# Optimization experiments

Measured on AMD Instinct MI355X. Metric: run time of the kernel, lower is better.

Reference implementation:

```python
import jax, jax.numpy as jnp
from jax import lax
import numpy as np

N, D, K = 262144, 256, 32


def setup_inputs() -> dict:
    key = jax.random.key(0)
    k1, k2 = jax.random.split(key)
    inputs = jax.random.normal(k1, (N, D), dtype=jnp.float32)
    q_vectors = jax.random.normal(k2, (K, D), dtype=jnp.float32)
    return {"inputs": inputs, "q_vectors": q_vectors}


def reference(inputs, q_vectors):
    # Sequence of Householder reflections: x <- x - (x @ q) outer (2/||q||^2 q)
    squared_norms = jnp.sum(q_vectors ** 2, axis=-1)  # [K]

    def step(x, qn):
        q, sq = qn  # q: [D], sq: scalar
        coeff = x @ q  # [N]
        x = x - jnp.outer(coeff, (2.0 / sq) * q)  # rank-1 update, [N, D]
        return x, None

    outputs, _ = lax.scan(step, inputs, (q_vectors, squared_norms))
    logabsdet = jnp.zeros(inputs.shape[0], dtype=inputs.dtype)
    return outputs, logabsdet
```

## Files before the change

kernel.cpp:

```cpp
#include <hip/hip_runtime.h>

#define N_ROWS 262144
#define DDIM   256
#define KREF   32

typedef __attribute__((ext_vector_type(4))) float f32x4;
typedef __attribute__((ext_vector_type(8))) short bf16x8;

__device__ bf16x8 g_Vhi[2 * 8 * 64];
__device__ bf16x8 g_Vlo[2 * 8 * 64];
__device__ bf16x8 g_Uhi[16 * 64];
__device__ bf16x8 g_Ulo[16 * 64];

__device__ __forceinline__ unsigned short f2bf(float x) {
    unsigned u = __float_as_uint(x);
    u += 0x7fffu + ((u >> 16) & 1u);
    return (unsigned short)(u >> 16);
}
__device__ __forceinline__ float bf2f(unsigned short h) {
    return __uint_as_float(((unsigned)h) << 16);
}

#define QS_LD 264
#define T_LD  33
#define U_LD  36

__global__ __launch_bounds__(256)
void setup_kernel(const float* __restrict__ Q) {
    __shared__ float Qs[32 * QS_LD];
    __shared__ float G[32 * 32];
    __shared__ float T[32 * T_LD];
    __shared__ float beta[32];
    __shared__ float U[256 * U_LD];
    const int tid = threadIdx.x;

    {
        const int q  = tid >> 3;
        const int c8 = tid & 7;
        const f32x4* src = (const f32x4*)(Q + q * DDIM);
        f32x4* dst = (f32x4*)(Qs + q * QS_LD);
        #pragma unroll
        for (int i = 0; i < 8; ++i)
            dst[c8 + 8 * i] = src[c8 + 8 * i];
    }
    __syncthreads();

    for (int p = tid; p < 1024; p += 256) {
        const int i = p >> 5, j = p & 31;
        const f32x4* qi = (const f32x4*)(Qs + i * QS_LD);
        const f32x4* qj = (const f32x4*)(Qs + j * QS_LD);
        float s = 0.f;
        #pragma unroll 8
        for (int d = 0; d < 64; ++d) {
            const f32x4 a = qi[d], b = qj[d];
            s += a.x * b.x + a.y * b.y + a.z * b.z + a.w * b.w;
        }
        G[p] = s;
    }
    for (int p = tid; p < 32 * T_LD; p += 256) T[p] = 0.f;
    __syncthreads();

    if (tid < 32) beta[tid] = 2.0f / G[tid * 32 + tid];
    __syncthreads();

    for (int k = 0; k < 32; ++k) {
        if (tid < k) {
            float s = 0.f;
            for (int j = tid; j < k; ++j) s += T[tid * T_LD + j] * G[j * 32 + k];
            T[tid * T_LD + k] = -beta[k] * s;
        } else if (tid == k) {
            T[k * T_LD + k] = beta[k];
        }
        __syncthreads();
    }

    for (int p = tid; p < 256 * 32; p += 256) {
        const int d = p >> 5, k = p & 31;
        float s = 0.f;
        for (int j = k; j < 32; ++j) s += T[k * T_LD + j] * Qs[j * QS_LD + d];
        U[d * U_LD + k] = s;
    }
    __syncthreads();

    for (int e = tid; e < 2 * 8 * 64; e += 256) {
        const int lane = e & 63, c = (e >> 6) & 7, nt = e >> 9;
        const int q  = 16 * nt + (lane & 15);
        const int d0 = 32 * c + 8 * (lane >> 4);
        bf16x8 vh, vl;
        #pragma unroll
        for (int j = 0; j < 8; ++j) {
            const float x = Qs[q * QS_LD + d0 + j];
            const unsigned short h = f2bf(x);
            vh[j] = (short)h;
            vl[j] = (short)f2bf(x - bf2f(h));
        }
        g_Vhi[e] = vh; g_Vlo[e] = vl;
    }
    for (int e = tid; e < 16 * 64; e += 256) {
        const int lane = e & 63, mt = e >> 6;
        const int d  = 16 * mt + (lane & 15);
        const int k0 = 8 * (lane >> 4);
        bf16x8 uh, ul;
        #pragma unroll
        for (int j = 0; j < 8; ++j) {
            const float x = U[d * U_LD + k0 + j];
            const unsigned short h = f2bf(x);
            uh[j] = (short)h;
            ul[j] = (short)f2bf(x - bf2f(h));
        }
        g_Uhi[e] = uh; g_Ulo[e] = ul;
    }
}

__global__ __launch_bounds__(256)
void wy_kernel(const float* __restrict__ X, float* __restrict__ out) {
    __shared__ float tlds[4 * 16 * 36];

    const int tid  = threadIdx.x;
    const int wave = tid >> 6;
    const int lane = tid & 63;
    const int t = lane & 15;
    const int g = lane >> 4;

    const size_t row0 = (size_t)blockIdx.x * 64 + wave * 16;

    const float* xp = X + (row0 + t) * DDIM + 8 * g;
    f32x4 xa[16];
    #pragma unroll
    for (int c = 0; c < 8; ++c) {
        xa[2 * c]     = *(const f32x4*)(xp + 32 * c);
        xa[2 * c + 1] = *(const f32x4*)(xp + 32 * c + 4);
    }

    bf16x8 ahi[8], alo[8];
    #pragma unroll
    for (int c = 0; c < 8; ++c) {
        #pragma unroll
        for (int e = 0; e < 8; ++e) {
            const float x = (e < 4) ? xa[2 * c][e] : xa[2 * c + 1][e - 4];
            const unsigned short h = f2bf(x);
            ahi[c][e] = (short)h;
            alo[c][e] = (short)f2bf(x - bf2f(h));
        }
    }

    f32x4 acc0 = {0.f, 0.f, 0.f, 0.f};
    f32x4 acc1 = {0.f, 0.f, 0.f, 0.f};
    #pragma unroll
    for (int c = 0; c < 8; ++c) {
        const bf16x8 bh0 = g_Vhi[c * 64 + lane];
        const bf16x8 bl0 = g_Vlo[c * 64 + lane];
        const bf16x8 bh1 = g_Vhi[512 + c * 64 + lane];
        const bf16x8 bl1 = g_Vlo[512 + c * 64 + lane];
        acc0 = __builtin_amdgcn_mfma_f32_16x16x32_bf16(ahi[c], bh0, acc0, 0, 0, 0);
        acc0 = __builtin_amdgcn_mfma_f32_16x16x32_bf16(alo[c], bh0, acc0, 0, 0, 0);
        acc0 = __builtin_amdgcn_mfma_f32_16x16x32_bf16(ahi[c], bl0, acc0, 0, 0, 0);
        acc1 = __builtin_amdgcn_mfma_f32_16x16x32_bf16(ahi[c], bh1, acc1, 0, 0, 0);
        acc1 = __builtin_amdgcn_mfma_f32_16x16x32_bf16(alo[c], bh1, acc1, 0, 0, 0);
        acc1 = __builtin_amdgcn_mfma_f32_16x16x32_bf16(ahi[c], bl1, acc1, 0, 0, 0);
    }

    const float* xr = X + (row0 + t) * DDIM + 4 * g;
    f32x4 xe[16];
    #pragma unroll
    for (int mt = 0; mt < 16; ++mt)
        xe[mt] = *(const f32x4*)(xr + 16 * mt);

    float* tb = tlds + wave * (16 * 36);
    #pragma unroll
    for (int r = 0; r < 4; ++r) {
        tb[(4 * g + r) * 36 + t]      = acc0[r];
        tb[(4 * g + r) * 36 + 16 + t] = acc1[r];
    }
    asm volatile("s_waitcnt lgkmcnt(0)" ::: "memory");
    const f32x4 c01 = *(const f32x4*)(tb + t * 36 + 8 * g);
    const f32x4 c23 = *(const f32x4*)(tb + t * 36 + 8 * g + 4);

    bf16x8 chi, clo;
    #pragma unroll
    for (int j = 0; j < 8; ++j) {
        const float v = -((j < 4) ? c01[j] : c23[j - 4]);
        const unsigned short h = f2bf(v);
        chi[j] = (short)h;
        clo[j] = (short)f2bf(v - bf2f(h));
    }

    float* op = out + (row0 + t) * DDIM + 4 * g;
    #pragma unroll
    for (int mt = 0; mt < 16; ++mt) {
        const bf16x8 uh = g_Uhi[mt * 64 + lane];
        const bf16x8 ul = g_Ulo[mt * 64 + lane];
        f32x4 a = xe[mt];
        a = __builtin_amdgcn_mfma_f32_16x16x32_bf16(uh, chi, a, 0, 0, 0);
        a = __builtin_amdgcn_mfma_f32_16x16x32_bf16(ul, chi, a, 0, 0, 0);
        a = __builtin_amdgcn_mfma_f32_16x16x32_bf16(uh, clo, a, 0, 0, 0);
        __builtin_nontemporal_store(a, (f32x4*)(op + 16 * mt));
    }

    if (tid < 64)
        out[(size_t)N_ROWS * DDIM + (size_t)blockIdx.x * 64 + tid] = 0.0f;
}

extern "C" void kernel_launch(void* const* d_in, const int* in_sizes, int n_in,
                              void* d_out, int out_size, void* d_ws, size_t ws_size,
                              hipStream_t stream) {
    const float* X = (const float*)d_in[0];
    const float* Q = (const float*)d_in[1];
    float* out = (float*)d_out;

    setup_kernel<<<1, 256, 0, stream>>>(Q);
    wy_kernel<<<N_ROWS / 64, 256, 0, stream>>>(X, out);
}
```

Baseline: 567.8 us.

## Split setup into two kernels, multi-tile WY blocks with LDS-staged V and prefetch

The single-block setup kernel is split in two: the first builds T and the V fragments, and the second computes U = T·Q in parallel across 16 blocks. The main kernel now handles four 64-row tiles per block. It stages the V fragments in LDS once per block and prefetches the next tile's X while converting the current one. It also splits the MFMA accumulators into hi and lo chains to shorten dependency chains, sets a launch bound of 2 blocks per CU, and switches output stores from nontemporal to regular. The aim is to cut serial setup latency and per-block overhead, at the cost of higher register and LDS use and one extra launch.

New measurement: 524.0 us. -7.7%, faster.

```diff
diff --git a/kernel.cpp b/kernel.cpp
--- a/kernel.cpp
+++ b/kernel.cpp
@@ -3,6 +3,8 @@
 #define N_ROWS 262144
 #define DDIM   256
 #define KREF   32
+#define TILES  4
+#define GRID_WY (N_ROWS / (64 * TILES))
 
 typedef __attribute__((ext_vector_type(4))) float f32x4;
 typedef __attribute__((ext_vector_type(8))) short bf16x8;
@@ -11,6 +13,7 @@
 __device__ bf16x8 g_Vlo[2 * 8 * 64];
 __device__ bf16x8 g_Uhi[16 * 64];
 __device__ bf16x8 g_Ulo[16 * 64];
+__device__ float  g_T[32 * 32];
 
 __device__ __forceinline__ unsigned short f2bf(float x) {
     unsigned u = __float_as_uint(x);
@@ -23,15 +26,13 @@
 
 #define QS_LD 264
 #define T_LD  33
-#define U_LD  36
 
 __global__ __launch_bounds__(256)
-void setup_kernel(const float* __restrict__ Q) {
+void setup_a(const float* __restrict__ Q) {
     __shared__ float Qs[32 * QS_LD];
     __shared__ float G[32 * 32];
     __shared__ float T[32 * T_LD];
     __shared__ float beta[32];
-    __shared__ float U[256 * U_LD];
     const int tid = threadIdx.x;
 
     {
@@ -74,13 +75,8 @@
         __syncthreads();
     }
 
-    for (int p = tid; p < 256 * 32; p += 256) {
-        const int d = p >> 5, k = p & 31;
-        float s = 0.f;
-        for (int j = k; j < 32; ++j) s += T[k * T_LD + j] * Qs[j * QS_LD + d];
-        U[d * U_LD + k] = s;
-    }
-    __syncthreads();
+    for (int p = tid; p < 1024; p += 256)
+        g_T[p] = T[(p >> 5) * T_LD + (p & 31)];
 
     for (int e = tid; e < 2 * 8 * 64; e += 256) {
         const int lane = e & 63, c = (e >> 6) & 7, nt = e >> 9;
@@ -96,25 +92,49 @@
         }
         g_Vhi[e] = vh; g_Vlo[e] = vl;
     }
-    for (int e = tid; e < 16 * 64; e += 256) {
-        const int lane = e & 63, mt = e >> 6;
-        const int d  = 16 * mt + (lane & 15);
-        const int k0 = 8 * (lane >> 4);
+}
+
+__global__ __launch_bounds__(256)
+void setup_b(const float* __restrict__ Q) {
+    __shared__ float Ts[32 * 32];
+    __shared__ float Us[16 * 33];
+    const int tid = threadIdx.x;
+    const int m = blockIdx.x;
+
+    for (int p = tid; p < 1024; p += 256) Ts[p] = g_T[p];
+    __syncthreads();
+
+    #pragma unroll
+    for (int e = 0; e < 2; ++e) {
+        const int idx = tid + 256 * e;
+        const int dd = idx >> 5, k = idx & 31;
+        const int d = 16 * m + dd;
+        float s = 0.f;
+        for (int j = k; j < 32; ++j) s += Ts[k * 32 + j] * Q[j * DDIM + d];
+        Us[dd * 33 + k] = s;
+    }
+    __syncthreads();
+
+    if (tid < 64) {
+        const int dd = tid & 15, k0 = 8 * (tid >> 4);
         bf16x8 uh, ul;
         #pragma unroll
         for (int j = 0; j < 8; ++j) {
-            const float x = U[d * U_LD + k0 + j];
+            const float x = Us[dd * 33 + k0 + j];
             const unsigned short h = f2bf(x);
             uh[j] = (short)h;
             ul[j] = (short)f2bf(x - bf2f(h));
         }
-        g_Uhi[e] = uh; g_Ulo[e] = ul;
-    }
-}
-
-__global__ __launch_bounds__(256)
+        g_Uhi[m * 64 + tid] = uh;
+        g_Ulo[m * 64 + tid] = ul;
+    }
+}
+
+__global__ __launch_bounds__(256, 2)
 void wy_kernel(const float* __restrict__ X, float* __restrict__ out) {
-    __shared__ float tlds[4 * 16 * 36];
+    __shared__ bf16x8 sVhi[1024];
+    __shared__ bf16x8 sVlo[1024];
+    __shared__ float  tscr[4 * 16 * 36];
 
     const int tid  = threadIdx.x;
     const int wave = tid >> 6;
@@ -122,83 +142,113 @@
     const int t = lane & 15;
     const int g = lane >> 4;
 
-    const size_t row0 = (size_t)blockIdx.x * 64 + wave * 16;
-
-    const float* xp = X + (row0 + t) * DDIM + 8 * g;
+    {
+        const f32x4* s1 = (const f32x4*)g_Vhi;
+        const f32x4* s2 = (const f32x4*)g_Vlo;
+        f32x4* d1 = (f32x4*)sVhi;
+        f32x4* d2 = (f32x4*)sVlo;
+        #pragma unroll
+        for (int i = 0; i < 4; ++i) {
+            d1[tid + 256 * i] = s1[tid + 256 * i];
+            d2[tid + 256 * i] = s2[tid + 256 * i];
+        }
+    }
+    __syncthreads();
+
+    const size_t base = (size_t)blockIdx.x * (64 * TILES) + wave * 16 + t;
+    float* tb = tscr + wave * (16 * 36);
+
     f32x4 xa[16];
+    {
+        const float* xp = X + base * DDIM + 8 * g;
+        #pragma unroll
+        for (int c = 0; c < 8; ++c) {
+            xa[2 * c]     = *(const f32x4*)(xp + 32 * c);
+            xa[2 * c + 1] = *(const f32x4*)(xp + 32 * c + 4);
+        }
+    }
+
     #pragma unroll
-    for (int c = 0; c < 8; ++c) {
-        xa[2 * c]     = *(const f32x4*)(xp + 32 * c);
-        xa[2 * c + 1] = *(const f32x4*)(xp + 32 * c + 4);
-    }
-
-    bf16x8 ahi[8], alo[8];
-    #pragma unroll
-    for (int c = 0; c < 8; ++c) {
-        #pragma unroll
-        for (int e = 0; e < 8; ++e) {
-            const float x = (e < 4) ? xa[2 * c][e] : xa[2 * c + 1][e - 4];
-            const unsigned short h = f2bf(x);
-            ahi[c][e] = (short)h;
-            alo[c][e] = (short)f2bf(x - bf2f(h));
-        }
-    }
-
-    f32x4 acc0 = {0.f, 0.f, 0.f, 0.f};
-    f32x4 acc1 = {0.f, 0.f, 0.f, 0.f};
-    #pragma unroll
-    for (int c = 0; c < 8; ++c) {
-        const bf16x8 bh0 = g_Vhi[c * 64 + lane];
-        const bf16x8 bl0 = g_Vlo[c * 64 + lane];
-        const bf16x8 bh1 = g_Vhi[512 + c * 64 + lane];
-        const bf16x8 bl1 = g_Vlo[512 + c * 64 + lane];
-        acc0 = __builtin_amdgcn_mfma_f32_16x16x32_bf16(ahi[c], bh0, acc0, 0, 0, 0);
-        acc0 = __builtin_amdgcn_mfma_f32_16x16x32_bf16(alo[c], bh0, acc0, 0, 0, 0);
-        acc0 = __builtin_amdgcn_mfma_f32_16x16x32_bf16(ahi[c], bl0, acc0, 0, 0, 0);
-        acc1 = __builtin_amdgcn_mfma_f32_16x16x32_bf16(ahi[c], bh1, acc1, 0, 0, 0);
-        acc1 = __builtin_amdgcn_mfma_f32_16x16x32_bf16(alo[c], bh1, acc1, 0, 0, 0);
-        acc1 = __builtin_amdgcn_mfma_f32_16x16x32_bf16(ahi[c], bl1, acc1, 0, 0, 0);
-    }
-
-    const float* xr = X + (row0 + t) * DDIM + 4 * g;
-    f32x4 xe[16];
-    #pragma unroll
-    for (int mt = 0; mt < 16; ++mt)
-        xe[mt] = *(const f32x4*)(xr + 16 * mt);
-
-    float* tb = tlds + wave * (16 * 36);
-    #pragma unroll
-    for (int r = 0; r < 4; ++r) {
-        tb[(4 * g + r) * 36 + t]      = acc0[r];
-        tb[(4 * g + r) * 36 + 16 + t] = acc1[r];
-    }
-    asm volatile("s_waitcnt lgkmcnt(0)" ::: "memory");
-    const f32x4 c01 = *(const f32x4*)(tb + t * 36 + 8 * g);
-    const f32x4 c23 = *(const f32x4*)(tb + t * 36 + 8 * g + 4);
-
-    bf16x8 chi, clo;
-    #pragma unroll
-    for (int j = 0; j < 8; ++j) {
-        const float v = -((j < 4) ? c01[j] : c23[j - 4]);
-        const unsigned short h = f2bf(v);
-        chi[j] = (short)h;
-        clo[j] = (short)f2bf(v - bf2f(h));
-    }
-
-    float* op = out + (row0 + t) * DDIM + 4 * g;
-    #pragma unroll
-    for (int mt = 0; mt < 16; ++mt) {
-        const bf16x8 uh = g_Uhi[mt * 64 + lane];
-        const bf16x8 ul = g_Ulo[mt * 64 + lane];
-        f32x4 a = xe[mt];
-        a = __builtin_amdgcn_mfma_f32_16x16x32_bf16(uh, chi, a, 0, 0, 0);
-        a = __builtin_amdgcn_mfma_f32_16x16x32_bf16(ul, chi, a, 0, 0, 0);
-        a = __builtin_amdgcn_mfma_f32_16x16x32_bf16(uh, clo, a, 0, 0, 0);
-        __builtin_nontemporal_store(a, (f32x4*)(op + 16 * mt));
-    }
-
-    if (tid < 64)
-        out[(size_t)N_ROWS * DDIM + (size_t)blockIdx.x * 64 + tid] = 0.0f;
+    for (int tt = 0; tt < TILES; ++tt) {
+        const size_t row = base + (size_t)tt * 64;
+
+        bf16x8 ahi[8], alo[8];
+        #pragma unroll
+        for (int c = 0; c < 8; ++c) {
+            #pragma unroll
+            for (int e = 0; e < 8; ++e) {
+                const float x = (e < 4) ? xa[2 * c][e] : xa[2 * c + 1][e - 4];
+                const unsigned short h = f2bf(x);
+                ahi[c][e] = (short)h;
+                alo[c][e] = (short)f2bf(x - bf2f(h));
+            }
+        }
+
+        if (tt + 1 < TILES) {
+            const float* xp = X + (row + 64) * DDIM + 8 * g;
+            #pragma unroll
+            for (int c = 0; c < 8; ++c) {
+                xa[2 * c]     = *(const f32x4*)(xp + 32 * c);
+                xa[2 * c + 1] = *(const f32x4*)(xp + 32 * c + 4);
+            }
+        }
+
+        f32x4 a0h = {0.f, 0.f, 0.f, 0.f}, a0l = {0.f, 0.f, 0.f, 0.f};
+        f32x4 a1h = {0.f, 0.f, 0.f, 0.f}, a1l = {0.f, 0.f, 0.f, 0.f};
+        #pragma unroll
+        for (int c = 0; c < 8; ++c) {
+            const bf16x8 bh0 = sVhi[c * 64 + lane];
+            const bf16x8 bl0 = sVlo[c * 64 + lane];
+            const bf16x8 bh1 = sVhi[512 + c * 64 + lane];
+            const bf16x8 bl1 = sVlo[512 + c * 64 + lane];
+            a0h = __builtin_amdgcn_mfma_f32_16x16x32_bf16(ahi[c], bh0, a0h, 0, 0, 0);
+            a0l = __builtin_amdgcn_mfma_f32_16x16x32_bf16(alo[c], bh0, a0l, 0, 0, 0);
+            a0l = __builtin_amdgcn_mfma_f32_16x16x32_bf16(ahi[c], bl0, a0l, 0, 0, 0);
+            a1h = __builtin_amdgcn_mfma_f32_16x16x32_bf16(ahi[c], bh1, a1h, 0, 0, 0);
+            a1l = __builtin_amdgcn_mfma_f32_16x16x32_bf16(alo[c], bh1, a1l, 0, 0, 0);
+            a1l = __builtin_amdgcn_mfma_f32_16x16x32_bf16(ahi[c], bl1, a1l, 0, 0, 0);
+        }
+        const f32x4 acc0 = a0h + a0l;
+        const f32x4 acc1 = a1h + a1l;
+
+        f32x4 xe[16];
+        const float* xr = X + row * DDIM + 4 * g;
+        #pragma unroll
+        for (int mt = 0; mt < 16; ++mt)
+            xe[mt] = *(const f32x4*)(xr + 16 * mt);
+
+        #pragma unroll
+        for (int r = 0; r < 4; ++r) {
+            tb[(4 * g + r) * 36 + t]      = acc0[r];
+            tb[(4 * g + r) * 36 + 16 + t] = acc1[r];
+        }
+        asm volatile("s_waitcnt lgkmcnt(0)" ::: "memory");
+        const f32x4 c01 = *(const f32x4*)(tb + t * 36 + 8 * g);
+        const f32x4 c23 = *(const f32x4*)(tb + t * 36 + 8 * g + 4);
+
+        bf16x8 chi, clo;
+        #pragma unroll
+        for (int j = 0; j < 8; ++j) {
+            const float v = -((j < 4) ? c01[j] : c23[j - 4]);
+            const unsigned short h = f2bf(v);
+            chi[j] = (short)h;
+            clo[j] = (short)f2bf(v - bf2f(h));
+        }
+
+        float* op = out + row * DDIM + 4 * g;
+        #pragma unroll
+        for (int mt = 0; mt < 16; ++mt) {
+            const bf16x8 uh = g_Uhi[mt * 64 + lane];
+            const bf16x8 ul = g_Ulo[mt * 64 + lane];
+            f32x4 a = xe[mt];
+            a = __builtin_amdgcn_mfma_f32_16x16x32_bf16(uh, chi, a, 0, 0, 0);
+            a = __builtin_amdgcn_mfma_f32_16x16x32_bf16(ul, chi, a, 0, 0, 0);
+            a = __builtin_amdgcn_mfma_f32_16x16x32_bf16(uh, clo, a, 0, 0, 0);
+            *(f32x4*)(op + 16 * mt) = a;
+        }
+    }
+
+    out[(size_t)N_ROWS * DDIM + (size_t)blockIdx.x * 256 + tid] = 0.0f;
 }
 
 extern "C" void kernel_launch(void* const* d_in, const int* in_sizes, int n_in,
@@ -208,6 +258,7 @@
     const float* Q = (const float*)d_in[1];
     float* out = (float*)d_out;
 
-    setup_kernel<<<1, 256, 0, stream>>>(Q);
-    wy_kernel<<<N_ROWS / 64, 256, 0, stream>>>(X, out);
-}
+    setup_a<<<1, 256, 0, stream>>>(Q);
+    setup_b<<<16, 256, 0, stream>>>(Q);
+    wy_kernel<<<GRID_WY, 256, 0, stream>>>(X, out);
+}
```
